# Optimization experiments

Hardware: AMD Instinct MI355X
Metric: run time of the kernel (lower is better)

Reference implementation:

```python
import jax, jax.numpy as jnp
import numpy as np

# DeltaNet single-token decode step. Hard-coded dims from the torch source:
# hidden H=2048 (chosen), qk=2048 (16h x 128 -> repeat to 32h), v=4096 (32h x 128),
# conv channels 8192, kernel 4, state [1,32,128,128].
H = 2048
EPS = 1e-6

def _l2norm(x):
    return x * jax.lax.rsqrt(jnp.sum(x * x, axis=-1, keepdims=True) + EPS)

def setup_inputs() -> dict:
    key = jax.random.key(0)
    ks = jax.random.split(key, 12)
    w = lambda k, s, sc=0.02: jax.random.normal(k, s, dtype=jnp.float32) * sc
    return {
        "x": jax.random.normal(ks[0], (1, 1, H), dtype=jnp.float32),
        "state": jax.random.normal(ks[1], (1, 32, 128, 128), dtype=jnp.float32) * 0.02,
        "conv_state": jax.random.normal(ks[2], (1, 8192, 3), dtype=jnp.float32) * 0.1,
        "W_qkv": w(ks[3], (8192, H)),
        "W_z": w(ks[4], (4096, H)),
        "W_b": w(ks[5], (32, H)),
        "W_a": w(ks[6], (32, H)),
        "conv_w": w(ks[7], (8192, 1, 4), 0.3),
        "A_log": jax.random.uniform(ks[8], (32,), minval=-2.0, maxval=0.0, dtype=jnp.float32),
        "dt_bias": w(ks[9], (32,), 0.5),
        "norm_w": jnp.ones((128,), jnp.float32),
        "W_out": w(ks[10], (H, 4096)),
    }

def reference(x, state, conv_state, W_qkv, W_z, W_b, W_a, conv_w, A_log, dt_bias, norm_w, W_out):
    # projections (bias-free Linear, torch convention y = x @ W.T)
    mixed = jnp.einsum('blh,ch->blc', x, W_qkv)           # [1,1,8192]
    z = jnp.einsum('blh,ch->blc', x, W_z).reshape(1, 1, 32, 128)
    beta = jax.nn.sigmoid(jnp.einsum('blh,ch->blc', x, W_b))  # [1,1,32]
    a = jnp.einsum('blh,ch->blc', x, W_a)                 # [1,1,32]

    # depthwise causal conv (groups=8192, kernel 4, output length 1)
    combined = jnp.concatenate([conv_state, mixed.transpose(0, 2, 1)], axis=-1)  # [1,8192,4]
    new_conv = combined[:, :, -3:]
    conv_out = jnp.sum(combined * conv_w[None, :, 0, :], axis=-1)  # [1,8192]
    mixed = jax.nn.silu(conv_out)[:, None, :]             # [1,1,8192]

    q, k, v = mixed[..., :2048], mixed[..., 2048:4096], mixed[..., 4096:]
    q = jnp.repeat(q.reshape(1, 1, 16, 128), 2, axis=2)   # [1,1,32,128]
    k = jnp.repeat(k.reshape(1, 1, 16, 128), 2, axis=2)
    v = v.reshape(1, 1, 32, 128)

    g = -jnp.exp(A_log) * jax.nn.softplus(a + dt_bias)    # [1,1,32]

    q = _l2norm(q)[:, 0] / jnp.sqrt(jnp.float32(128.0))   # [1,32,128]
    k = _l2norm(k)[:, 0]
    v = v[:, 0]
    g_t = jnp.exp(g[:, 0])[..., None, None]               # [1,32,1,1]
    beta_t = beta[:, 0][..., None]                        # [1,32,1]

    # gated delta-rule state update
    s = state * g_t                                       # [1,32,128,128]
    kv_mem = jnp.einsum('bhkv,bhk->bhv', s, k)            # [1,32,128]
    delta = (v - kv_mem) * beta_t
    new_state = s + k[..., None] * delta[..., None, :]    # [1,32,128,128]
    out = jnp.einsum('bhkv,bhk->bhv', new_state, q)       # [1,32,128]

    # gated RMSNorm (Mamba2-style: rmsnorm(x * silu(z)) * w)
    out_flat = out.reshape(-1, 128)
    z_flat = z.reshape(-1, 128)
    gated = out_flat * jax.nn.silu(z_flat)
    out_flat = gated * jax.lax.rsqrt(jnp.mean(gated * gated, axis=-1, keepdims=True) + EPS) * norm_w

    out = jnp.einsum('blc,hc->blh', out_flat.reshape(1, 1, 4096), W_out)  # [1,1,H]
    return (out, new_state, new_conv)
```

## Files before the change

kernel.cpp:

```cpp
#include <hip/hip_runtime.h>
#include <math.h>

__global__ __launch_bounds__(256) void k_gemv_in(
    const float* __restrict__ x,
    const float* __restrict__ Wqkv,
    const float* __restrict__ Wz,
    const float* __restrict__ Wb,
    const float* __restrict__ Wa,
    float* __restrict__ mixed, float* __restrict__ zb,
    float* __restrict__ b_raw, float* __restrict__ a_raw)
{
  const int tid  = threadIdx.x;
  const int lane = tid & 63;
  const int wave = tid >> 6;

  float4 xr[8];
  #pragma unroll
  for (int j = 0; j < 8; j++)
    xr[j] = *(const float4*)(x + j*256 + lane*4);

  const int row0 = blockIdx.x * 8 + wave * 2;
  const float* W; float* dst;
  if (row0 < 8192)       { W = Wqkv + (size_t)row0 * 2048;          dst = mixed + row0; }
  else if (row0 < 12288) { W = Wz   + (size_t)(row0-8192) * 2048;   dst = zb + (row0-8192); }
  else if (row0 < 12320) { W = Wb   + (size_t)(row0-12288) * 2048;  dst = b_raw + (row0-12288); }
  else                   { W = Wa   + (size_t)(row0-12320) * 2048;  dst = a_raw + (row0-12320); }

  float acc0 = 0.f, acc1 = 0.f;
  #pragma unroll
  for (int j = 0; j < 8; j++){
    float4 w0 = *(const float4*)(W + j*256 + lane*4);
    float4 w1 = *(const float4*)(W + 2048 + j*256 + lane*4);
    acc0 += w0.x*xr[j].x + w0.y*xr[j].y + w0.z*xr[j].z + w0.w*xr[j].w;
    acc1 += w1.x*xr[j].x + w1.y*xr[j].y + w1.z*xr[j].z + w1.w*xr[j].w;
  }
  #pragma unroll
  for (int off = 32; off >= 1; off >>= 1){
    acc0 += __shfl_xor(acc0, off, 64);
    acc1 += __shfl_xor(acc1, off, 64);
  }
  if (lane == 0){ dst[0] = acc0; dst[1] = acc1; }
}

__global__ __launch_bounds__(128) void k_head(
    const float* __restrict__ mixed,
    const float* __restrict__ conv_state,
    const float* __restrict__ conv_w,
    const float* __restrict__ zbuf,
    const float* __restrict__ b_raw,
    const float* __restrict__ a_raw,
    const float* __restrict__ A_log,
    const float* __restrict__ dt_bias,
    const float* __restrict__ norm_w,
    const float* __restrict__ state,
    float* __restrict__ new_state,
    float* __restrict__ new_conv,
    float* __restrict__ out_flat)
{
  const int h = blockIdx.x;
  const int t = threadIdx.x;
  const int hb = h >> 1;
  const int lane = t & 63, wid = t >> 6;

  __shared__ float qn[128], kn[128];
  __shared__ float red[4];

  const int cq = hb*128 + t;
  const int ck = 2048 + hb*128 + t;
  const int cv = 4096 + h*128 + t;
  float qv, kv, vv;
  {
    float c0, c1, c2, m, w0, w1, w2, w3, co;
    c0 = conv_state[cq*3+0]; c1 = conv_state[cq*3+1]; c2 = conv_state[cq*3+2];
    m  = mixed[cq];
    w0 = conv_w[cq*4+0]; w1 = conv_w[cq*4+1]; w2 = conv_w[cq*4+2]; w3 = conv_w[cq*4+3];
    co = c0*w0 + c1*w1 + c2*w2 + m*w3;
    qv = co / (1.f + expf(-co));
    new_conv[cq*3+0] = c1; new_conv[cq*3+1] = c2; new_conv[cq*3+2] = m;
    c0 = conv_state[ck*3+0]; c1 = conv_state[ck*3+1]; c2 = conv_state[ck*3+2];
    m  = mixed[ck];
    w0 = conv_w[ck*4+0]; w1 = conv_w[ck*4+1]; w2 = conv_w[ck*4+2]; w3 = conv_w[ck*4+3];
    co = c0*w0 + c1*w1 + c2*w2 + m*w3;
    kv = co / (1.f + expf(-co));
    new_conv[ck*3+0] = c1; new_conv[ck*3+1] = c2; new_conv[ck*3+2] = m;
    c0 = conv_state[cv*3+0]; c1 = conv_state[cv*3+1]; c2 = conv_state[cv*3+2];
    m  = mixed[cv];
    w0 = conv_w[cv*4+0]; w1 = conv_w[cv*4+1]; w2 = conv_w[cv*4+2]; w3 = conv_w[cv*4+3];
    co = c0*w0 + c1*w1 + c2*w2 + m*w3;
    vv = co / (1.f + expf(-co));
    new_conv[cv*3+0] = c1; new_conv[cv*3+1] = c2; new_conv[cv*3+2] = m;
  }

  float sq = qv*qv, sk = kv*kv;
  #pragma unroll
  for (int off = 32; off >= 1; off >>= 1){
    sq += __shfl_xor(sq, off, 64);
    sk += __shfl_xor(sk, off, 64);
  }
  if (lane == 0){ red[wid] = sq; red[2+wid] = sk; }
  __syncthreads();
  const float qscale = rsqrtf(red[0]+red[1] + 1e-6f) * 0.088388347648318440550f;
  const float kscale = rsqrtf(red[2]+red[3] + 1e-6f);
  qn[t] = qv * qscale;
  kn[t] = kv * kscale;
  __syncthreads();

  float g_t, beta;
  {
    const float av = a_raw[h] + dt_bias[h];
    const float sp = (av > 20.f) ? av : log1pf(expf(av));
    g_t  = expf(-expf(A_log[h]) * sp);
    beta = 1.f / (1.f + expf(-b_raw[h]));
  }

  const float* st  = state     + (size_t)h * 16384;
  float*       nst = new_state + (size_t)h * 16384;

  float s[128];
  float kvm = 0.f;
  #pragma unroll
  for (int k = 0; k < 128; k++){
    s[k] = st[k*128 + t] * g_t;
    kvm += s[k] * kn[k];
  }
  const float delta = (vv - kvm) * beta;
  float oacc = 0.f;
  #pragma unroll
  for (int k = 0; k < 128; k++){
    const float ns = s[k] + kn[k] * delta;
    nst[k*128 + t] = ns;
    oacc += ns * qn[k];
  }

  const float zz = zbuf[h*128 + t];
  const float gated = oacc * (zz / (1.f + expf(-zz)));
  float s2 = gated * gated;
  #pragma unroll
  for (int off = 32; off >= 1; off >>= 1) s2 += __shfl_xor(s2, off, 64);
  if (lane == 0) red[wid] = s2;
  __syncthreads();
  const float mean = (red[0] + red[1]) * (1.f/128.f);
  out_flat[h*128 + t] = gated * rsqrtf(mean + 1e-6f) * norm_w[t];
}

__global__ __launch_bounds__(256) void k_gemv_out(
    const float* __restrict__ out_flat,
    const float* __restrict__ Wout,
    float* __restrict__ out)
{
  __shared__ float xs[4096];
  const int tid = threadIdx.x;
  #pragma unroll
  for (int i = 0; i < 4; i++)
    *(float4*)(xs + tid*4 + i*1024) = *(const float4*)(out_flat + tid*4 + i*1024);
  __syncthreads();

  const int lane = tid & 63, wave = tid >> 6;
  const int row0 = blockIdx.x * 8 + wave * 2;
  const float* W0 = Wout + (size_t)row0 * 4096;
  float acc0 = 0.f, acc1 = 0.f;
  #pragma unroll
  for (int j = 0; j < 16; j++){
    float4 w0 = *(const float4*)(W0 + j*256 + lane*4);
    float4 w1 = *(const float4*)(W0 + 4096 + j*256 + lane*4);
    const float x0 = xs[j*256+lane*4+0], x1 = xs[j*256+lane*4+1];
    const float x2 = xs[j*256+lane*4+2], x3 = xs[j*256+lane*4+3];
    acc0 += w0.x*x0 + w0.y*x1 + w0.z*x2 + w0.w*x3;
    acc1 += w1.x*x0 + w1.y*x1 + w1.z*x2 + w1.w*x3;
  }
  #pragma unroll
  for (int off = 32; off >= 1; off >>= 1){
    acc0 += __shfl_xor(acc0, off, 64);
    acc1 += __shfl_xor(acc1, off, 64);
  }
  if (lane == 0){ out[row0] = acc0; out[row0+1] = acc1; }
}

extern "C" void kernel_launch(void* const* d_in, const int* in_sizes, int n_in,
                              void* d_out, int out_size, void* d_ws, size_t ws_size,
                              hipStream_t stream) {
  const float* x          = (const float*)d_in[0];
  const float* state      = (const float*)d_in[1];
  const float* conv_state = (const float*)d_in[2];
  const float* W_qkv      = (const float*)d_in[3];
  const float* W_z        = (const float*)d_in[4];
  const float* W_b        = (const float*)d_in[5];
  const float* W_a        = (const float*)d_in[6];
  const float* conv_w     = (const float*)d_in[7];
  const float* A_log      = (const float*)d_in[8];
  const float* dt_bias    = (const float*)d_in[9];
  const float* norm_w     = (const float*)d_in[10];
  const float* W_out      = (const float*)d_in[11];

  float* out       = (float*)d_out;
  float* new_state = (float*)d_out + 2048;
  float* new_conv  = (float*)d_out + 2048 + 524288;

  float* ws     = (float*)d_ws;
  float* mixed  = ws;
  float* zb     = ws + 8192;
  float* b_raw  = ws + 12288;
  float* a_raw  = ws + 12320;
  float* oflat  = ws + 12352;

  hipLaunchKernelGGL(k_gemv_in, dim3(1544), dim3(256), 0, stream,
                     x, W_qkv, W_z, W_b, W_a, mixed, zb, b_raw, a_raw);
  hipLaunchKernelGGL(k_head, dim3(32), dim3(128), 0, stream,
                     mixed, conv_state, conv_w, zb, b_raw, a_raw, A_log, dt_bias,
                     norm_w, state, new_state, new_conv, oflat);
  hipLaunchKernelGGL(k_gemv_out, dim3(256), dim3(256), 0, stream,
                     oflat, W_out, out);
}
```

Baseline: 180.6 us.

## Widen head kernel to 256 threads and prefetch W_out in spare blocks

The per-head delta-rule kernel now uses 256 threads per head. Each thread updates a 16x4 slice of the state with float4 loads and stores, and partial kv_mem and output sums are reduced through shared memory, replacing the 128-register-per-thread serial loop. The q/k and v convolutions are split across the two thread halves. Extra blocks (32..255) are launched that stream most of W_out and write a dummy sum to scratch, so the following output GEMV finds those rows warm in cache. This adds extra blocks and shared-memory reductions, and the prefetch costs bandwidth that may compete with the state traffic.

```diff
diff --git a/kernel.cpp b/kernel.cpp
--- a/kernel.cpp
+++ b/kernel.cpp
@@ -1,5 +1,7 @@
 #include <hip/hip_runtime.h>
 #include <math.h>
+
+__device__ __forceinline__ float silu(float x){ return x / (1.f + expf(-x)); }
 
 __global__ __launch_bounds__(256) void k_gemv_in(
     const float* __restrict__ x,
@@ -42,7 +44,7 @@
   if (lane == 0){ dst[0] = acc0; dst[1] = acc1; }
 }
 
-__global__ __launch_bounds__(128) void k_head(
+__global__ __launch_bounds__(256) void k_head(
     const float* __restrict__ mixed,
     const float* __restrict__ conv_state,
     const float* __restrict__ conv_w,
@@ -53,56 +55,68 @@
     const float* __restrict__ dt_bias,
     const float* __restrict__ norm_w,
     const float* __restrict__ state,
+    const float* __restrict__ Wout,
     float* __restrict__ new_state,
     float* __restrict__ new_conv,
-    float* __restrict__ out_flat)
+    float* __restrict__ out_flat,
+    float* __restrict__ scratch)
 {
-  const int h = blockIdx.x;
-  const int t = threadIdx.x;
+  const int b   = blockIdx.x;
+  const int tid = threadIdx.x;
+
+  if (b >= 32){
+    const float4* W4 = (const float4*)Wout + (size_t)b * 8192;
+    float4 a = make_float4(0.f, 0.f, 0.f, 0.f);
+    #pragma unroll
+    for (int j = 0; j < 32; j++){
+      float4 w = W4[j*256 + tid];
+      a.x += w.x; a.y += w.y; a.z += w.z; a.w += w.w;
+    }
+    if (tid == 0) scratch[b] = a.x + a.y + a.z + a.w;
+    return;
+  }
+
+  const int h  = b;
   const int hb = h >> 1;
-  const int lane = t & 63, wid = t >> 6;
+  const int t  = tid & 127;
+  const int lane = tid & 63, wid = tid >> 6;
 
   __shared__ float qn[128], kn[128];
+  __shared__ __align__(16) float vs[128];
+  __shared__ float4 kvp[8][32];
   __shared__ float red[4];
 
-  const int cq = hb*128 + t;
-  const int ck = 2048 + hb*128 + t;
-  const int cv = 4096 + h*128 + t;
-  float qv, kv, vv;
-  {
-    float c0, c1, c2, m, w0, w1, w2, w3, co;
-    c0 = conv_state[cq*3+0]; c1 = conv_state[cq*3+1]; c2 = conv_state[cq*3+2];
-    m  = mixed[cq];
-    w0 = conv_w[cq*4+0]; w1 = conv_w[cq*4+1]; w2 = conv_w[cq*4+2]; w3 = conv_w[cq*4+3];
-    co = c0*w0 + c1*w1 + c2*w2 + m*w3;
-    qv = co / (1.f + expf(-co));
-    new_conv[cq*3+0] = c1; new_conv[cq*3+1] = c2; new_conv[cq*3+2] = m;
-    c0 = conv_state[ck*3+0]; c1 = conv_state[ck*3+1]; c2 = conv_state[ck*3+2];
-    m  = mixed[ck];
-    w0 = conv_w[ck*4+0]; w1 = conv_w[ck*4+1]; w2 = conv_w[ck*4+2]; w3 = conv_w[ck*4+3];
-    co = c0*w0 + c1*w1 + c2*w2 + m*w3;
-    kv = co / (1.f + expf(-co));
-    new_conv[ck*3+0] = c1; new_conv[ck*3+1] = c2; new_conv[ck*3+2] = m;
-    c0 = conv_state[cv*3+0]; c1 = conv_state[cv*3+1]; c2 = conv_state[cv*3+2];
-    m  = mixed[cv];
-    w0 = conv_w[cv*4+0]; w1 = conv_w[cv*4+1]; w2 = conv_w[cv*4+2]; w3 = conv_w[cv*4+3];
-    co = c0*w0 + c1*w1 + c2*w2 + m*w3;
-    vv = co / (1.f + expf(-co));
-    new_conv[cv*3+0] = c1; new_conv[cv*3+1] = c2; new_conv[cv*3+2] = m;
-  }
-
-  float sq = qv*qv, sk = kv*kv;
-  #pragma unroll
-  for (int off = 32; off >= 1; off >>= 1){
-    sq += __shfl_xor(sq, off, 64);
-    sk += __shfl_xor(sk, off, 64);
-  }
-  if (lane == 0){ red[wid] = sq; red[2+wid] = sk; }
+  float qv = 0.f, kv = 0.f;
+  if (tid < 128){
+    int c = hb*128 + t;
+    float c0 = conv_state[c*3+0], c1 = conv_state[c*3+1], c2 = conv_state[c*3+2];
+    float m  = mixed[c];
+    qv = silu(c0*conv_w[c*4+0] + c1*conv_w[c*4+1] + c2*conv_w[c*4+2] + m*conv_w[c*4+3]);
+    new_conv[c*3+0] = c1; new_conv[c*3+1] = c2; new_conv[c*3+2] = m;
+    c = 2048 + hb*128 + t;
+    c0 = conv_state[c*3+0]; c1 = conv_state[c*3+1]; c2 = conv_state[c*3+2];
+    m  = mixed[c];
+    kv = silu(c0*conv_w[c*4+0] + c1*conv_w[c*4+1] + c2*conv_w[c*4+2] + m*conv_w[c*4+3]);
+    new_conv[c*3+0] = c1; new_conv[c*3+1] = c2; new_conv[c*3+2] = m;
+
+    float sq = qv*qv, sk = kv*kv;
+    #pragma unroll
+    for (int off = 32; off >= 1; off >>= 1){
+      sq += __shfl_xor(sq, off, 64);
+      sk += __shfl_xor(sk, off, 64);
+    }
+    if (lane == 0){ red[wid] = sq; red[2+wid] = sk; }
+  } else {
+    int c = 4096 + h*128 + t;
+    float c0 = conv_state[c*3+0], c1 = conv_state[c*3+1], c2 = conv_state[c*3+2];
+    float m  = mixed[c];
+    vs[t] = silu(c0*conv_w[c*4+0] + c1*conv_w[c*4+1] + c2*conv_w[c*4+2] + m*conv_w[c*4+3]);
+    new_conv[c*3+0] = c1; new_conv[c*3+1] = c2; new_conv[c*3+2] = m;
+  }
   __syncthreads();
   const float qscale = rsqrtf(red[0]+red[1] + 1e-6f) * 0.088388347648318440550f;
   const float kscale = rsqrtf(red[2]+red[3] + 1e-6f);
-  qn[t] = qv * qscale;
-  kn[t] = kv * kscale;
+  if (tid < 128){ qn[t] = qv * qscale; kn[t] = kv * kscale; }
   __syncthreads();
 
   float g_t, beta;
@@ -113,34 +127,77 @@
     beta = 1.f / (1.f + expf(-b_raw[h]));
   }
 
+  const int cg = tid & 31, part = tid >> 5;
+  const int k0 = part * 16;
   const float* st  = state     + (size_t)h * 16384;
   float*       nst = new_state + (size_t)h * 16384;
 
-  float s[128];
-  float kvm = 0.f;
-  #pragma unroll
-  for (int k = 0; k < 128; k++){
-    s[k] = st[k*128 + t] * g_t;
-    kvm += s[k] * kn[k];
-  }
-  const float delta = (vv - kvm) * beta;
-  float oacc = 0.f;
-  #pragma unroll
-  for (int k = 0; k < 128; k++){
-    const float ns = s[k] + kn[k] * delta;
-    nst[k*128 + t] = ns;
-    oacc += ns * qn[k];
-  }
-
-  const float zz = zbuf[h*128 + t];
-  const float gated = oacc * (zz / (1.f + expf(-zz)));
-  float s2 = gated * gated;
-  #pragma unroll
-  for (int off = 32; off >= 1; off >>= 1) s2 += __shfl_xor(s2, off, 64);
-  if (lane == 0) red[wid] = s2;
-  __syncthreads();
-  const float mean = (red[0] + red[1]) * (1.f/128.f);
-  out_flat[h*128 + t] = gated * rsqrtf(mean + 1e-6f) * norm_w[t];
+  float4 s4[16];
+  float4 kvm = make_float4(0.f, 0.f, 0.f, 0.f);
+  #pragma unroll
+  for (int i = 0; i < 16; i++){
+    float4 sv = *(const float4*)(st + (k0+i)*128 + cg*4);
+    sv.x *= g_t; sv.y *= g_t; sv.z *= g_t; sv.w *= g_t;
+    s4[i] = sv;
+    const float kk = kn[k0+i];
+    kvm.x += sv.x*kk; kvm.y += sv.y*kk; kvm.z += sv.z*kk; kvm.w += sv.w*kk;
+  }
+  kvp[part][cg] = kvm;
+  __syncthreads();
+  float4 kt = make_float4(0.f, 0.f, 0.f, 0.f);
+  #pragma unroll
+  for (int p = 0; p < 8; p++){
+    float4 kp = kvp[p][cg];
+    kt.x += kp.x; kt.y += kp.y; kt.z += kp.z; kt.w += kp.w;
+  }
+  const float4 v4 = *(const float4*)(vs + cg*4);
+  float4 delta;
+  delta.x = (v4.x - kt.x) * beta;
+  delta.y = (v4.y - kt.y) * beta;
+  delta.z = (v4.z - kt.z) * beta;
+  delta.w = (v4.w - kt.w) * beta;
+
+  float4 oacc = make_float4(0.f, 0.f, 0.f, 0.f);
+  #pragma unroll
+  for (int i = 0; i < 16; i++){
+    const float kk = kn[k0+i];
+    float4 ns;
+    ns.x = s4[i].x + kk*delta.x;
+    ns.y = s4[i].y + kk*delta.y;
+    ns.z = s4[i].z + kk*delta.z;
+    ns.w = s4[i].w + kk*delta.w;
+    *(float4*)(nst + (k0+i)*128 + cg*4) = ns;
+    const float qq = qn[k0+i];
+    oacc.x += ns.x*qq; oacc.y += ns.y*qq; oacc.z += ns.z*qq; oacc.w += ns.w*qq;
+  }
+  __syncthreads();
+  kvp[part][cg] = oacc;
+  __syncthreads();
+  if (part == 0){
+    float4 o = make_float4(0.f, 0.f, 0.f, 0.f);
+    #pragma unroll
+    for (int p = 0; p < 8; p++){
+      float4 op = kvp[p][cg];
+      o.x += op.x; o.y += op.y; o.z += op.z; o.w += op.w;
+    }
+    const float4 z4 = *(const float4*)(zbuf + h*128 + cg*4);
+    float4 g4;
+    g4.x = o.x * silu(z4.x);
+    g4.y = o.y * silu(z4.y);
+    g4.z = o.z * silu(z4.z);
+    g4.w = o.w * silu(z4.w);
+    float s2 = g4.x*g4.x + g4.y*g4.y + g4.z*g4.z + g4.w*g4.w;
+    #pragma unroll
+    for (int off = 16; off >= 1; off >>= 1) s2 += __shfl_xor(s2, off, 64);
+    const float r = rsqrtf(s2 * (1.f/128.f) + 1e-6f);
+    const float4 nw = *(const float4*)(norm_w + cg*4);
+    float4 ov;
+    ov.x = g4.x * r * nw.x;
+    ov.y = g4.y * r * nw.y;
+    ov.z = g4.z * r * nw.z;
+    ov.w = g4.w * r * nw.w;
+    *(float4*)(out_flat + h*128 + cg*4) = ov;
+  }
 }
 
 __global__ __launch_bounds__(256) void k_gemv_out(
@@ -196,18 +253,19 @@
   float* new_state = (float*)d_out + 2048;
   float* new_conv  = (float*)d_out + 2048 + 524288;
 
-  float* ws     = (float*)d_ws;
-  float* mixed  = ws;
-  float* zb     = ws + 8192;
-  float* b_raw  = ws + 12288;
-  float* a_raw  = ws + 12320;
-  float* oflat  = ws + 12352;
+  float* ws      = (float*)d_ws;
+  float* mixed   = ws;
+  float* zb      = ws + 8192;
+  float* b_raw   = ws + 12288;
+  float* a_raw   = ws + 12320;
+  float* oflat   = ws + 12352;
+  float* scratch = ws + 16448;
 
   hipLaunchKernelGGL(k_gemv_in, dim3(1544), dim3(256), 0, stream,
                      x, W_qkv, W_z, W_b, W_a, mixed, zb, b_raw, a_raw);
-  hipLaunchKernelGGL(k_head, dim3(32), dim3(128), 0, stream,
+  hipLaunchKernelGGL(k_head, dim3(256), dim3(256), 0, stream,
                      mixed, conv_state, conv_w, zb, b_raw, a_raw, A_log, dt_bias,
-                     norm_w, state, new_state, new_conv, oflat);
+                     norm_w, state, W_out, new_state, new_conv, oflat, scratch);
   hipLaunchKernelGGL(k_gemv_out, dim3(256), dim3(256), 0, stream,
                      oflat, W_out, out);
 }
```

Measured after the change: 177.8 us. Within noise of the previous version (-1.5%).
